# Performance work log

Measured on AMD Instinct MI355X. Metric: run time of the kernel, lower is better.

Reference implementation:

```python
import jax, jax.numpy as jnp
import numpy as np
import math

C_S = 256
NUM_HEADS = 8
HEAD_DIM = 32
TOTAL = NUM_HEADS * HEAD_DIM
B, S, I = 1, 256, 256  # batch, msa sequences (column attn axis), residues
LN_EPS = 1e-5


def setup_inputs() -> dict:
    key = jax.random.key(0)
    ks = jax.random.split(key, 10)
    sc = 1.0 / math.sqrt(C_S)
    return {
        "msa": jax.random.normal(ks[0], (B, S, I, C_S), dtype=jnp.float32),
        "ln_gamma": jnp.ones((C_S,), dtype=jnp.float32),
        "ln_beta": jnp.zeros((C_S,), dtype=jnp.float32),
        "Wq": jax.random.normal(ks[1], (C_S, TOTAL), dtype=jnp.float32) * sc,
        "Wk": jax.random.normal(ks[2], (C_S, TOTAL), dtype=jnp.float32) * sc,
        "Wv": jax.random.normal(ks[3], (C_S, TOTAL), dtype=jnp.float32) * sc,
        "Wg": jax.random.normal(ks[4], (C_S, TOTAL), dtype=jnp.float32) * sc,
        "bg": jnp.zeros((TOTAL,), dtype=jnp.float32),
        "Wo": jax.random.normal(ks[5], (TOTAL, C_S), dtype=jnp.float32) * (1.0 / math.sqrt(TOTAL)),
        "bo": jnp.zeros((C_S,), dtype=jnp.float32),
    }


def reference(msa, ln_gamma, ln_beta, Wq, Wk, Wv, Wg, bg, Wo, bo):
    # LayerNorm over channel dim
    mu = jnp.mean(msa, axis=-1, keepdims=True)
    var = jnp.mean(jnp.square(msa - mu), axis=-1, keepdims=True)
    x = (msa - mu) * jax.lax.rsqrt(var + LN_EPS) * ln_gamma + ln_beta

    b, s, i, _ = x.shape
    hd = (NUM_HEADS, HEAD_DIM)
    Q = (x @ Wq).reshape(b, s, i, *hd)
    K = (x @ Wk).reshape(b, s, i, *hd)
    V = (x @ Wv).reshape(b, s, i, *hd)
    G = jax.nn.sigmoid((x @ Wg + bg).reshape(b, s, i, *hd))

    # column attention: contract over head_dim, attend over sequence axis s/t
    scores = jnp.einsum('bsihd,btihd->bihst', Q, K) / math.sqrt(HEAD_DIM)
    attn = jax.nn.softmax(scores, axis=-1)
    vals = jnp.einsum('bihst,btihd->bsihd', attn, V)

    vals = (G * vals).reshape(b, s, i, TOTAL)
    return vals @ Wo + bo
```

## Files before the change

### kernel.cpp

```cpp
#include <hip/hip_runtime.h>
#include <hip/hip_fp16.h>
#include <math.h>

#define C_S 256
#define NUM_HEADS 8
#define HEAD_DIM 32
#define TOTAL 256
#define S_DIM 256
#define I_DIM 256
#define NROWS (S_DIM * I_DIM)
#define LN_EPS 1e-5f
#define QSCALE 0.25503534f

typedef _Float16 f16x8 __attribute__((ext_vector_type(8)));
typedef __attribute__((ext_vector_type(4))) float f32x4;

__device__ __forceinline__ ushort f2h(float x) {
  return __half_as_ushort(__float2half(x));
}
__device__ __forceinline__ float h2f(ushort u) {
  return __half2float(__ushort_as_half(u));
}
__device__ __forceinline__ uint pkrtz(float a, float b) {
  return __builtin_bit_cast(uint, __builtin_amdgcn_cvt_pkrtz(a, b));
}
__device__ __forceinline__ void gl16(const void* g, void* l) {
  __builtin_amdgcn_global_load_lds(
      (const __attribute__((address_space(1))) unsigned*)g,
      (__attribute__((address_space(3))) unsigned*)l, 16, 0, 0);
}
__device__ __forceinline__ void quadx(uint x0, uint x1, uint& o0, uint& o1) {
  auto a = __builtin_amdgcn_permlane32_swap(x0, x1, false, false);
  auto b = __builtin_amdgcn_permlane16_swap(a[0], a[1], false, false);
  o0 = b[0]; o1 = b[1];
}

__global__ __launch_bounds__(256) void prep_w_kernel(
    const float* __restrict__ Wq, const float* __restrict__ Wk,
    const float* __restrict__ Wv, const float* __restrict__ Wg,
    const float* __restrict__ Wo,
    ushort* __restrict__ Wch, ushort* __restrict__ Woh) {
  const int b = blockIdx.x;
  const int mat = b >> 8, n = b & 255;
  const int k = threadIdx.x;
  const float* W = (mat == 0) ? Wq : (mat == 1) ? Wk
                  : (mat == 2) ? Wv : (mat == 3) ? Wg : Wo;
  ushort h = f2h(W[(size_t)k * 256 + n]);
  if (mat < 4) Wch[((size_t)(mat * 256 + n)) * 256 + k] = h;
  else         Woh[(size_t)n * 256 + k] = h;
}

__global__ __launch_bounds__(256) void prep_x_kernel(
    const float* __restrict__ msa, const float* __restrict__ gamma,
    const float* __restrict__ beta, ushort* __restrict__ Xh) {
  const int row  = blockIdx.x * 4 + (threadIdx.x >> 6);
  const int lane = threadIdx.x & 63;
  float4 v = ((const float4*)(msa + (size_t)row * C_S))[lane];
  float sum = v.x + v.y + v.z + v.w;
  float sq  = v.x*v.x + v.y*v.y + v.z*v.z + v.w*v.w;
  #pragma unroll
  for (int off = 1; off < 64; off <<= 1) {
    sum += __shfl_xor(sum, off);
    sq  += __shfl_xor(sq, off);
  }
  float mu = sum * (1.0f / 256.0f);
  float rs = rsqrtf(sq * (1.0f / 256.0f) - mu * mu + LN_EPS);
  float4 gv = ((const float4*)gamma)[lane];
  float4 bv = ((const float4*)beta)[lane];
  ushort4 hh;
  hh.x = f2h((v.x - mu) * rs * gv.x + bv.x);
  hh.y = f2h((v.y - mu) * rs * gv.y + bv.y);
  hh.z = f2h((v.z - mu) * rs * gv.z + bv.z);
  hh.w = f2h((v.w - mu) * rs * gv.w + bv.w);
  *(ushort4*)(Xh + (size_t)row * 256 + lane * 4) = hh;
}

__global__ __launch_bounds__(256, 3) void fused_attn_kernel(
    const ushort* __restrict__ Xh,
    const ushort* __restrict__ Wch,
    const float* __restrict__ bg,
    ushort* __restrict__ Oh) {
  __shared__ __align__(16) ushort Kls[256][40];
  __shared__ __align__(16) ushort Vth[32][264];

  const int bid = blockIdx.x;
  const int xcd = bid & 7, j = bid >> 3;
  const int h = j & 7;
  const int i = (xcd << 5) + (j >> 3);
  const int ih = i * NUM_HEADS + h;
  const int tid = threadIdx.x;
  const int wave = tid >> 6, lane = tid & 63;
  const int lr = lane & 15, quad = lane >> 4;
  const int s_base = wave * 64;
  const size_t hbase = (size_t)ih * (S_DIM * HEAD_DIM);

  const ushort* xr0 = Xh + ((size_t)(s_base + lr) * 256 + i) * 256 + quad * 8;
  const ushort* wr0 = Wch + ((size_t)(h * 32 + lr)) * 256 + quad * 8;

  f32x4 kacc[2][4] = {}, vacc[2][4] = {};
  #pragma unroll
  for (int kb = 0; kb < 8; ++kb) {
    f16x8 xb[4];
    #pragma unroll
    for (int nt = 0; nt < 4; ++nt)
      xb[nt] = *(const f16x8*)(xr0 + (size_t)nt * 16 * 65536 + kb * 32);
    f16x8 wk[2], wv[2];
    #pragma unroll
    for (int mt = 0; mt < 2; ++mt) {
      wk[mt] = *(const f16x8*)(wr0 + (size_t)1 * 65536 + mt * 4096 + kb * 32);
      wv[mt] = *(const f16x8*)(wr0 + (size_t)2 * 65536 + mt * 4096 + kb * 32);
    }
    #pragma unroll
    for (int mt = 0; mt < 2; ++mt)
      #pragma unroll
      for (int nt = 0; nt < 4; ++nt) {
        kacc[mt][nt] = __builtin_amdgcn_mfma_f32_16x16x32_f16(wk[mt], xb[nt], kacc[mt][nt], 0, 0, 0);
        vacc[mt][nt] = __builtin_amdgcn_mfma_f32_16x16x32_f16(xb[nt], wv[mt], vacc[mt][nt], 0, 0, 0);
      }
  }
  #pragma unroll
  for (int mt = 0; mt < 2; ++mt)
    #pragma unroll
    for (int nt = 0; nt < 4; ++nt) {
      const int t = s_base + nt * 16 + lr;
      ushort4 kp;
      kp.x = f2h(kacc[mt][nt][0]); kp.y = f2h(kacc[mt][nt][1]);
      kp.z = f2h(kacc[mt][nt][2]); kp.w = f2h(kacc[mt][nt][3]);
      *(ushort4*)&Kls[t][mt * 16 + quad * 4] = kp;
      ushort4 vp;
      vp.x = f2h(vacc[mt][nt][0]); vp.y = f2h(vacc[mt][nt][1]);
      vp.z = f2h(vacc[mt][nt][2]); vp.w = f2h(vacc[mt][nt][3]);
      *(ushort4*)&Vth[mt * 16 + lr][s_base + nt * 16 + quad * 4] = vp;
    }

  f32x4 qacc[2][4] = {}, gacc[2][4] = {};
  #pragma unroll
  for (int kb = 0; kb < 8; ++kb) {
    f16x8 xb[4];
    #pragma unroll
    for (int nt = 0; nt < 4; ++nt)
      xb[nt] = *(const f16x8*)(xr0 + (size_t)nt * 16 * 65536 + kb * 32);
    f16x8 wq[2], wg[2];
    #pragma unroll
    for (int mt = 0; mt < 2; ++mt) {
      wq[mt] = *(const f16x8*)(wr0 + (size_t)0 * 65536 + mt * 4096 + kb * 32);
      wg[mt] = *(const f16x8*)(wr0 + (size_t)3 * 65536 + mt * 4096 + kb * 32);
    }
    #pragma unroll
    for (int mt = 0; mt < 2; ++mt)
      #pragma unroll
      for (int nt = 0; nt < 4; ++nt) {
        qacc[mt][nt] = __builtin_amdgcn_mfma_f32_16x16x32_f16(wq[mt], xb[nt], qacc[mt][nt], 0, 0, 0);
        gacc[mt][nt] = __builtin_amdgcn_mfma_f32_16x16x32_f16(wg[mt], xb[nt], gacc[mt][nt], 0, 0, 0);
      }
  }
  f16x8 qf[4];
  #pragma unroll
  for (int ns = 0; ns < 4; ++ns) {
    uint x0 = (uint)f2h(qacc[0][ns][0] * QSCALE) | ((uint)f2h(qacc[0][ns][1] * QSCALE) << 16);
    uint y0 = (uint)f2h(qacc[0][ns][2] * QSCALE) | ((uint)f2h(qacc[0][ns][3] * QSCALE) << 16);
    uint x1 = (uint)f2h(qacc[1][ns][0] * QSCALE) | ((uint)f2h(qacc[1][ns][1] * QSCALE) << 16);
    uint y1 = (uint)f2h(qacc[1][ns][2] * QSCALE) | ((uint)f2h(qacc[1][ns][3] * QSCALE) << 16);
    uint qa, qb, qc, qd2;
    quadx(x0, x1, qa, qb);
    quadx(y0, y1, qc, qd2);
    uint4 qw4 = make_uint4(qa, qc, qb, qd2);
    qf[ns] = __builtin_bit_cast(f16x8, qw4);
  }

  __syncthreads();

  f32x4 oacc[2][4] = {};
  float lpart[4] = {};
  #pragma unroll 1
  for (int c = 0; c < 4; ++c) {
    const int t0 = c * 64;
    #pragma unroll
    for (int half = 0; half < 2; ++half) {
      f16x8 kf0 = *(const f16x8*)&Kls[t0 + (half * 2 + 0) * 16 + lr][quad * 8];
      f16x8 kf1 = *(const f16x8*)&Kls[t0 + (half * 2 + 1) * 16 + lr][quad * 8];
      const int tq = t0 + half * 32 + quad * 8;
      f16x8 v0 = *(const f16x8*)&Vth[lr][tq];
      f16x8 v1 = *(const f16x8*)&Vth[16 + lr][tq];
      #pragma unroll
      for (int ns = 0; ns < 4; ++ns) {
        f32x4 s0 = {}, s1 = {};
        s0 = __builtin_amdgcn_mfma_f32_16x16x32_f16(kf0, qf[ns], s0, 0, 0, 0);
        s1 = __builtin_amdgcn_mfma_f32_16x16x32_f16(kf1, qf[ns], s1, 0, 0, 0);
        float e00 = exp2f(s0[0]), e01 = exp2f(s0[1]);
        float e02 = exp2f(s0[2]), e03 = exp2f(s0[3]);
        float e10 = exp2f(s1[0]), e11 = exp2f(s1[1]);
        float e12 = exp2f(s1[2]), e13 = exp2f(s1[3]);
        lpart[ns] += ((e00 + e01) + (e02 + e03)) + ((e10 + e11) + (e12 + e13));
        uint x0 = pkrtz(e00, e01), y0 = pkrtz(e02, e03);
        uint x1 = pkrtz(e10, e11), y1 = pkrtz(e12, e13);
        uint pa, pb, pc, pd;
        quadx(x0, x1, pa, pb);
        quadx(y0, y1, pc, pd);
        uint4 pw4 = make_uint4(pa, pc, pb, pd);
        f16x8 pf = __builtin_bit_cast(f16x8, pw4);
        __builtin_amdgcn_s_setprio(1);
        oacc[0][ns] = __builtin_amdgcn_mfma_f32_16x16x32_f16(v0, pf, oacc[0][ns], 0, 0, 0);
        oacc[1][ns] = __builtin_amdgcn_mfma_f32_16x16x32_f16(v1, pf, oacc[1][ns], 0, 0, 0);
        __builtin_amdgcn_s_setprio(0);
      }
    }
  }

  float invl[4];
  #pragma unroll
  for (int ns = 0; ns < 4; ++ns) {
    float v = lpart[ns];
    v += __shfl_xor(v, 16);
    v += __shfl_xor(v, 32);
    invl[ns] = 1.0f / v;
  }

  #pragma unroll
  for (int ns = 0; ns < 4; ++ns) {
    const int s = s_base + ns * 16 + lr;
    #pragma unroll
    for (int md = 0; md < 2; ++md) {
      const int d0 = md * 16 + quad * 4;
      float4 bgv = *(const float4*)(bg + h * 32 + d0);
      float g0 = 1.0f / (1.0f + __expf(-(gacc[md][ns][0] + bgv.x)));
      float g1 = 1.0f / (1.0f + __expf(-(gacc[md][ns][1] + bgv.y)));
      float g2 = 1.0f / (1.0f + __expf(-(gacc[md][ns][2] + bgv.z)));
      float g3 = 1.0f / (1.0f + __expf(-(gacc[md][ns][3] + bgv.w)));
      ushort4 ov;
      ov.x = f2h(g0 * oacc[md][ns][0] * invl[ns]);
      ov.y = f2h(g1 * oacc[md][ns][1] * invl[ns]);
      ov.z = f2h(g2 * oacc[md][ns][2] * invl[ns]);
      ov.w = f2h(g3 * oacc[md][ns][3] * invl[ns]);
      *(ushort4*)(Oh + hbase + (size_t)s * HEAD_DIM + d0) = ov;
    }
  }
}

__global__ __launch_bounds__(256) void out_kernel(
    const ushort* __restrict__ Oh, const ushort* __restrict__ Woh,
    const float* __restrict__ bo, float* __restrict__ out) {
  __shared__ __align__(16) ushort At0[128 * 32];
  __shared__ __align__(16) ushort At1[128 * 32];
  __shared__ __align__(16) ushort Bt0[128 * 32];
  __shared__ __align__(16) ushort Bt1[128 * 32];

  const int bid = blockIdx.x;
  const int xcd = bid & 7;
  const int j   = bid >> 3;
  const int ntile = j & 1;
  const int rg    = (xcd << 6) + (j >> 1);
  const int n0 = ntile * 128;
  const int s  = rg >> 1;
  const int i0 = (rg & 1) * 128;
  const int tid = threadIdx.x;
  const int wave = tid >> 6, lane = tid & 63;
  const int wm = wave >> 1, wn = wave & 1;
  const int lr = lane & 15, quad = lane >> 4;
  const int fsw = (quad ^ ((lr >> 1) & 3)) * 8;

  const int slot = wave * 64 + lane;
  const int row0 = slot >> 2;
  const int kc   = ((slot & 3) ^ ((row0 >> 1) & 3)) * 8;

  const ushort* pA = Oh + (size_t)(i0 + row0) * 65536 + (size_t)s * 32 + kc;
  const ushort* pB = Woh + (size_t)(n0 + row0) * 256 + kc;
  const int ld0 = wave * 512;
  const int ld1 = 2048 + wave * 512;

  f32x4 acc[4][4] = {};

  for (int kk = 0; kk < 4; ++kk) {
    __syncthreads();
    gl16(pA,               At0 + ld0); gl16(pA + (size_t)64 * 65536,        At0 + ld1);
    gl16(pA + 8192,        At1 + ld0); gl16(pA + (size_t)64 * 65536 + 8192, At1 + ld1);
    gl16(pB,               Bt0 + ld0); gl16(pB + 64 * 256,                  Bt0 + ld1);
    gl16(pB + 32,          Bt1 + ld0); gl16(pB + 64 * 256 + 32,             Bt1 + ld1);
    pA += 16384;
    pB += 64;
    __syncthreads();

    f16x8 a0[4], a1[4], b0[4], b1[4];
    #pragma unroll
    for (int mt = 0; mt < 4; ++mt) {
      const int off = (wm * 64 + mt * 16 + lr) * 32 + fsw;
      a0[mt] = *(const f16x8*)&At0[off];
      a1[mt] = *(const f16x8*)&At1[off];
    }
    #pragma unroll
    for (int nt = 0; nt < 4; ++nt) {
      const int off = (wn * 64 + nt * 16 + lr) * 32 + fsw;
      b0[nt] = *(const f16x8*)&Bt0[off];
      b1[nt] = *(const f16x8*)&Bt1[off];
    }
    #pragma unroll
    for (int mt = 0; mt < 4; ++mt)
      #pragma unroll
      for (int nt = 0; nt < 4; ++nt) {
        acc[mt][nt] = __builtin_amdgcn_mfma_f32_16x16x32_f16(a0[mt], b0[nt], acc[mt][nt], 0, 0, 0);
        acc[mt][nt] = __builtin_amdgcn_mfma_f32_16x16x32_f16(a1[mt], b1[nt], acc[mt][nt], 0, 0, 0);
      }
  }

  #pragma unroll
  for (int nt = 0; nt < 4; ++nt) {
    const int col = n0 + wn * 64 + nt * 16 + lr;
    const float b = bo[col];
    #pragma unroll
    for (int mt = 0; mt < 4; ++mt)
      #pragma unroll
      for (int reg = 0; reg < 4; ++reg) {
        const int mloc = wm * 64 + mt * 16 + quad * 4 + reg;
        out[((size_t)s * 256 + i0 + mloc) * C_S + col] = acc[mt][nt][reg] + b;
      }
  }
}

extern "C" void kernel_launch(void* const* d_in, const int* in_sizes, int n_in,
                              void* d_out, int out_size, void* d_ws, size_t ws_size,
                              hipStream_t stream) {
  const float* msa   = (const float*)d_in[0];
  const float* gamma = (const float*)d_in[1];
  const float* beta  = (const float*)d_in[2];
  const float* Wq    = (const float*)d_in[3];
  const float* Wk    = (const float*)d_in[4];
  const float* Wv    = (const float*)d_in[5];
  const float* Wg    = (const float*)d_in[6];
  const float* bg    = (const float*)d_in[7];
  const float* Wo    = (const float*)d_in[8];
  const float* bo    = (const float*)d_in[9];
  float* out = (float*)d_out;

  const size_t PLANE = (size_t)NROWS * TOTAL;
  ushort* Oh  = (ushort*)d_ws;
  ushort* Wch = Oh + PLANE;
  ushort* Woh = Wch + 1024 * 256;
  ushort* Xh = (ushort*)d_out;

  prep_w_kernel<<<1280, 256, 0, stream>>>(Wq, Wk, Wv, Wg, Wo, Wch, Woh);
  prep_x_kernel<<<NROWS / 4, 256, 0, stream>>>(msa, gamma, beta, Xh);
  fused_attn_kernel<<<I_DIM * NUM_HEADS, 256, 0, stream>>>(Xh, Wch, bg, Oh);
  out_kernel<<<1024, 256, 0, stream>>>(Oh, Woh, bo, out);
}
```

Baseline: 286.2 us.

## Spill sigmoid gate to global scratch to cut registers and raise occupancy

After: 289.8 us. No clear change (+1.3%).

```diff
diff --git a/kernel.cpp b/kernel.cpp
--- a/kernel.cpp
+++ b/kernel.cpp
@@ -75,11 +75,12 @@
   *(ushort4*)(Xh + (size_t)row * 256 + lane * 4) = hh;
 }
 
-__global__ __launch_bounds__(256, 3) void fused_attn_kernel(
+__global__ __launch_bounds__(256, 4) void fused_attn_kernel(
     const ushort* __restrict__ Xh,
     const ushort* __restrict__ Wch,
     const float* __restrict__ bg,
-    ushort* __restrict__ Oh) {
+    ushort* __restrict__ Oh,
+    ushort* __restrict__ Gh) {
   __shared__ __align__(16) ushort Kls[256][40];
   __shared__ __align__(16) ushort Vth[32][264];
 
@@ -97,75 +98,94 @@
   const ushort* xr0 = Xh + ((size_t)(s_base + lr) * 256 + i) * 256 + quad * 8;
   const ushort* wr0 = Wch + ((size_t)(h * 32 + lr)) * 256 + quad * 8;
 
-  f32x4 kacc[2][4] = {}, vacc[2][4] = {};
-  #pragma unroll
-  for (int kb = 0; kb < 8; ++kb) {
-    f16x8 xb[4];
-    #pragma unroll
-    for (int nt = 0; nt < 4; ++nt)
-      xb[nt] = *(const f16x8*)(xr0 + (size_t)nt * 16 * 65536 + kb * 32);
-    f16x8 wk[2], wv[2];
+  {
+    f32x4 kacc[2][4] = {}, vacc[2][4] = {};
+    #pragma unroll
+    for (int kb = 0; kb < 8; ++kb) {
+      f16x8 xb[4];
+      #pragma unroll
+      for (int nt = 0; nt < 4; ++nt)
+        xb[nt] = *(const f16x8*)(xr0 + (size_t)nt * 16 * 65536 + kb * 32);
+      f16x8 wk[2], wv[2];
+      #pragma unroll
+      for (int mt = 0; mt < 2; ++mt) {
+        wk[mt] = *(const f16x8*)(wr0 + (size_t)1 * 65536 + mt * 4096 + kb * 32);
+        wv[mt] = *(const f16x8*)(wr0 + (size_t)2 * 65536 + mt * 4096 + kb * 32);
+      }
+      #pragma unroll
+      for (int mt = 0; mt < 2; ++mt)
+        #pragma unroll
+        for (int nt = 0; nt < 4; ++nt) {
+          kacc[mt][nt] = __builtin_amdgcn_mfma_f32_16x16x32_f16(wk[mt], xb[nt], kacc[mt][nt], 0, 0, 0);
+          vacc[mt][nt] = __builtin_amdgcn_mfma_f32_16x16x32_f16(xb[nt], wv[mt], vacc[mt][nt], 0, 0, 0);
+        }
+    }
+    #pragma unroll
+    for (int mt = 0; mt < 2; ++mt)
+      #pragma unroll
+      for (int nt = 0; nt < 4; ++nt) {
+        const int t = s_base + nt * 16 + lr;
+        ushort4 kp;
+        kp.x = f2h(kacc[mt][nt][0]); kp.y = f2h(kacc[mt][nt][1]);
+        kp.z = f2h(kacc[mt][nt][2]); kp.w = f2h(kacc[mt][nt][3]);
+        *(ushort4*)&Kls[t][mt * 16 + quad * 4] = kp;
+        ushort4 vp;
+        vp.x = f2h(vacc[mt][nt][0]); vp.y = f2h(vacc[mt][nt][1]);
+        vp.z = f2h(vacc[mt][nt][2]); vp.w = f2h(vacc[mt][nt][3]);
+        *(ushort4*)&Vth[mt * 16 + lr][s_base + nt * 16 + quad * 4] = vp;
+      }
+  }
+
+  f16x8 qf[4];
+  {
+    f32x4 qacc[2][4] = {}, gacc[2][4] = {};
+    #pragma unroll
+    for (int kb = 0; kb < 8; ++kb) {
+      f16x8 xb[4];
+      #pragma unroll
+      for (int nt = 0; nt < 4; ++nt)
+        xb[nt] = *(const f16x8*)(xr0 + (size_t)nt * 16 * 65536 + kb * 32);
+      f16x8 wq[2], wg[2];
+      #pragma unroll
+      for (int mt = 0; mt < 2; ++mt) {
+        wq[mt] = *(const f16x8*)(wr0 + (size_t)0 * 65536 + mt * 4096 + kb * 32);
+        wg[mt] = *(const f16x8*)(wr0 + (size_t)3 * 65536 + mt * 4096 + kb * 32);
+      }
+      #pragma unroll
+      for (int mt = 0; mt < 2; ++mt)
+        #pragma unroll
+        for (int nt = 0; nt < 4; ++nt) {
+          qacc[mt][nt] = __builtin_amdgcn_mfma_f32_16x16x32_f16(wq[mt], xb[nt], qacc[mt][nt], 0, 0, 0);
+          gacc[mt][nt] = __builtin_amdgcn_mfma_f32_16x16x32_f16(wg[mt], xb[nt], gacc[mt][nt], 0, 0, 0);
+        }
+    }
     #pragma unroll
     for (int mt = 0; mt < 2; ++mt) {
-      wk[mt] = *(const f16x8*)(wr0 + (size_t)1 * 65536 + mt * 4096 + kb * 32);
-      wv[mt] = *(const f16x8*)(wr0 + (size_t)2 * 65536 + mt * 4096 + kb * 32);
-    }
-    #pragma unroll
-    for (int mt = 0; mt < 2; ++mt)
+      const int d0 = mt * 16 + quad * 4;
+      float4 bgv = *(const float4*)(bg + h * 32 + d0);
       #pragma unroll
       for (int nt = 0; nt < 4; ++nt) {
-        kacc[mt][nt] = __builtin_amdgcn_mfma_f32_16x16x32_f16(wk[mt], xb[nt], kacc[mt][nt], 0, 0, 0);
-        vacc[mt][nt] = __builtin_amdgcn_mfma_f32_16x16x32_f16(xb[nt], wv[mt], vacc[mt][nt], 0, 0, 0);
-      }
-  }
-  #pragma unroll
-  for (int mt = 0; mt < 2; ++mt)
-    #pragma unroll
-    for (int nt = 0; nt < 4; ++nt) {
-      const int t = s_base + nt * 16 + lr;
-      ushort4 kp;
-      kp.x = f2h(kacc[mt][nt][0]); kp.y = f2h(kacc[mt][nt][1]);
-      kp.z = f2h(kacc[mt][nt][2]); kp.w = f2h(kacc[mt][nt][3]);
-      *(ushort4*)&Kls[t][mt * 16 + quad * 4] = kp;
-      ushort4 vp;
-      vp.x = f2h(vacc[mt][nt][0]); vp.y = f2h(vacc[mt][nt][1]);
-      vp.z = f2h(vacc[mt][nt][2]); vp.w = f2h(vacc[mt][nt][3]);
-      *(ushort4*)&Vth[mt * 16 + lr][s_base + nt * 16 + quad * 4] = vp;
-    }
-
-  f32x4 qacc[2][4] = {}, gacc[2][4] = {};
-  #pragma unroll
-  for (int kb = 0; kb < 8; ++kb) {
-    f16x8 xb[4];
-    #pragma unroll
-    for (int nt = 0; nt < 4; ++nt)
-      xb[nt] = *(const f16x8*)(xr0 + (size_t)nt * 16 * 65536 + kb * 32);
-    f16x8 wq[2], wg[2];
-    #pragma unroll
-    for (int mt = 0; mt < 2; ++mt) {
-      wq[mt] = *(const f16x8*)(wr0 + (size_t)0 * 65536 + mt * 4096 + kb * 32);
-      wg[mt] = *(const f16x8*)(wr0 + (size_t)3 * 65536 + mt * 4096 + kb * 32);
-    }
-    #pragma unroll
-    for (int mt = 0; mt < 2; ++mt)
-      #pragma unroll
-      for (int nt = 0; nt < 4; ++nt) {
-        qacc[mt][nt] = __builtin_amdgcn_mfma_f32_16x16x32_f16(wq[mt], xb[nt], qacc[mt][nt], 0, 0, 0);
-        gacc[mt][nt] = __builtin_amdgcn_mfma_f32_16x16x32_f16(wg[mt], xb[nt], gacc[mt][nt], 0, 0, 0);
-      }
-  }
-  f16x8 qf[4];
-  #pragma unroll
-  for (int ns = 0; ns < 4; ++ns) {
-    uint x0 = (uint)f2h(qacc[0][ns][0] * QSCALE) | ((uint)f2h(qacc[0][ns][1] * QSCALE) << 16);
-    uint y0 = (uint)f2h(qacc[0][ns][2] * QSCALE) | ((uint)f2h(qacc[0][ns][3] * QSCALE) << 16);
-    uint x1 = (uint)f2h(qacc[1][ns][0] * QSCALE) | ((uint)f2h(qacc[1][ns][1] * QSCALE) << 16);
-    uint y1 = (uint)f2h(qacc[1][ns][2] * QSCALE) | ((uint)f2h(qacc[1][ns][3] * QSCALE) << 16);
-    uint qa, qb, qc, qd2;
-    quadx(x0, x1, qa, qb);
-    quadx(y0, y1, qc, qd2);
-    uint4 qw4 = make_uint4(qa, qc, qb, qd2);
-    qf[ns] = __builtin_bit_cast(f16x8, qw4);
+        const int s = s_base + nt * 16 + lr;
+        ushort4 gp;
+        gp.x = f2h(1.0f / (1.0f + __expf(-(gacc[mt][nt][0] + bgv.x))));
+        gp.y = f2h(1.0f / (1.0f + __expf(-(gacc[mt][nt][1] + bgv.y))));
+        gp.z = f2h(1.0f / (1.0f + __expf(-(gacc[mt][nt][2] + bgv.z))));
+        gp.w = f2h(1.0f / (1.0f + __expf(-(gacc[mt][nt][3] + bgv.w))));
+        *(ushort4*)(Gh + hbase + (size_t)s * HEAD_DIM + d0) = gp;
+      }
+    }
+    #pragma unroll
+    for (int ns = 0; ns < 4; ++ns) {
+      uint x0 = (uint)f2h(qacc[0][ns][0] * QSCALE) | ((uint)f2h(qacc[0][ns][1] * QSCALE) << 16);
+      uint y0 = (uint)f2h(qacc[0][ns][2] * QSCALE) | ((uint)f2h(qacc[0][ns][3] * QSCALE) << 16);
+      uint x1 = (uint)f2h(qacc[1][ns][0] * QSCALE) | ((uint)f2h(qacc[1][ns][1] * QSCALE) << 16);
+      uint y1 = (uint)f2h(qacc[1][ns][2] * QSCALE) | ((uint)f2h(qacc[1][ns][3] * QSCALE) << 16);
+      uint qa, qb, qc, qd2;
+      quadx(x0, x1, qa, qb);
+      quadx(y0, y1, qc, qd2);
+      uint4 qw4 = make_uint4(qa, qc, qb, qd2);
+      qf[ns] = __builtin_bit_cast(f16x8, qw4);
+    }
   }
 
   __syncthreads();
@@ -199,10 +219,8 @@
         quadx(y0, y1, pc, pd);
         uint4 pw4 = make_uint4(pa, pc, pb, pd);
         f16x8 pf = __builtin_bit_cast(f16x8, pw4);
-        __builtin_amdgcn_s_setprio(1);
         oacc[0][ns] = __builtin_amdgcn_mfma_f32_16x16x32_f16(v0, pf, oacc[0][ns], 0, 0, 0);
         oacc[1][ns] = __builtin_amdgcn_mfma_f32_16x16x32_f16(v1, pf, oacc[1][ns], 0, 0, 0);
-        __builtin_amdgcn_s_setprio(0);
       }
     }
   }
@@ -222,16 +240,12 @@
     #pragma unroll
     for (int md = 0; md < 2; ++md) {
       const int d0 = md * 16 + quad * 4;
-      float4 bgv = *(const float4*)(bg + h * 32 + d0);
-      float g0 = 1.0f / (1.0f + __expf(-(gacc[md][ns][0] + bgv.x)));
-      float g1 = 1.0f / (1.0f + __expf(-(gacc[md][ns][1] + bgv.y)));
-      float g2 = 1.0f / (1.0f + __expf(-(gacc[md][ns][2] + bgv.z)));
-      float g3 = 1.0f / (1.0f + __expf(-(gacc[md][ns][3] + bgv.w)));
+      ushort4 g4 = *(const ushort4*)(Gh + hbase + (size_t)s * HEAD_DIM + d0);
       ushort4 ov;
-      ov.x = f2h(g0 * oacc[md][ns][0] * invl[ns]);
-      ov.y = f2h(g1 * oacc[md][ns][1] * invl[ns]);
-      ov.z = f2h(g2 * oacc[md][ns][2] * invl[ns]);
-      ov.w = f2h(g3 * oacc[md][ns][3] * invl[ns]);
+      ov.x = f2h(h2f(g4.x) * oacc[md][ns][0] * invl[ns]);
+      ov.y = f2h(h2f(g4.y) * oacc[md][ns][1] * invl[ns]);
+      ov.z = f2h(h2f(g4.z) * oacc[md][ns][2] * invl[ns]);
+      ov.w = f2h(h2f(g4.w) * oacc[md][ns][3] * invl[ns]);
       *(ushort4*)(Oh + hbase + (size_t)s * HEAD_DIM + d0) = ov;
     }
   }
@@ -336,9 +350,10 @@
   ushort* Wch = Oh + PLANE;
   ushort* Woh = Wch + 1024 * 256;
   ushort* Xh = (ushort*)d_out;
+  ushort* Gh = Xh + PLANE;
 
   prep_w_kernel<<<1280, 256, 0, stream>>>(Wq, Wk, Wv, Wg, Wo, Wch, Woh);
   prep_x_kernel<<<NROWS / 4, 256, 0, stream>>>(msa, gamma, beta, Xh);
-  fused_attn_kernel<<<I_DIM * NUM_HEADS, 256, 0, stream>>>(Xh, Wch, bg, Oh);
+  fused_attn_kernel<<<I_DIM * NUM_HEADS, 256, 0, stream>>>(Xh, Wch, bg, Oh, Gh);
   out_kernel<<<1024, 256, 0, stream>>>(Oh, Woh, bo, out);
 }
```

## Double-buffer LDS loads in output projection GEMM with async prefetch

Applied to the files above, without the earlier changes.

After: 281.8 us. About the same (-1.5%).

```diff
diff --git a/kernel.cpp b/kernel.cpp
--- a/kernel.cpp
+++ b/kernel.cpp
@@ -240,10 +240,8 @@
 __global__ __launch_bounds__(256) void out_kernel(
     const ushort* __restrict__ Oh, const ushort* __restrict__ Woh,
     const float* __restrict__ bo, float* __restrict__ out) {
-  __shared__ __align__(16) ushort At0[128 * 32];
-  __shared__ __align__(16) ushort At1[128 * 32];
-  __shared__ __align__(16) ushort Bt0[128 * 32];
-  __shared__ __align__(16) ushort Bt1[128 * 32];
+  __shared__ __align__(16) ushort As[2][128 * 32];
+  __shared__ __align__(16) ushort Bs[2][128 * 32];
 
   const int bid = blockIdx.x;
   const int xcd = bid & 7;
@@ -270,37 +268,45 @@
 
   f32x4 acc[4][4] = {};
 
-  for (int kk = 0; kk < 4; ++kk) {
-    __syncthreads();
-    gl16(pA,               At0 + ld0); gl16(pA + (size_t)64 * 65536,        At0 + ld1);
-    gl16(pA + 8192,        At1 + ld0); gl16(pA + (size_t)64 * 65536 + 8192, At1 + ld1);
-    gl16(pB,               Bt0 + ld0); gl16(pB + 64 * 256,                  Bt0 + ld1);
-    gl16(pB + 32,          Bt1 + ld0); gl16(pB + 64 * 256 + 32,             Bt1 + ld1);
-    pA += 16384;
-    pB += 64;
-    __syncthreads();
-
-    f16x8 a0[4], a1[4], b0[4], b1[4];
-    #pragma unroll
-    for (int mt = 0; mt < 4; ++mt) {
-      const int off = (wm * 64 + mt * 16 + lr) * 32 + fsw;
-      a0[mt] = *(const f16x8*)&At0[off];
-      a1[mt] = *(const f16x8*)&At1[off];
-    }
-    #pragma unroll
-    for (int nt = 0; nt < 4; ++nt) {
-      const int off = (wn * 64 + nt * 16 + lr) * 32 + fsw;
-      b0[nt] = *(const f16x8*)&Bt0[off];
-      b1[nt] = *(const f16x8*)&Bt1[off];
-    }
+  #define STAGE(buf, kk)                                                     \
+    do {                                                                     \
+      const ushort* a_ = pA + (size_t)(kk) * 8192;                           \
+      const ushort* b_ = pB + (kk) * 32;                                     \
+      gl16(a_,                      As[buf] + ld0);                          \
+      gl16(a_ + (size_t)64 * 65536, As[buf] + ld1);                          \
+      gl16(b_,                      Bs[buf] + ld0);                          \
+      gl16(b_ + 64 * 256,           Bs[buf] + ld1);                          \
+    } while (0)
+
+  STAGE(0, 0);
+  int cur = 0;
+  #pragma unroll 1
+  for (int kk = 0; kk < 8; ++kk) {
+    if (kk < 7) {
+      STAGE(cur ^ 1, kk + 1);
+      asm volatile("s_waitcnt vmcnt(4)" ::: "memory");
+    } else {
+      asm volatile("s_waitcnt vmcnt(0)" ::: "memory");
+    }
+    __builtin_amdgcn_s_barrier();
+
+    f16x8 a0[4], b0[4];
     #pragma unroll
     for (int mt = 0; mt < 4; ++mt)
-      #pragma unroll
-      for (int nt = 0; nt < 4; ++nt) {
+      a0[mt] = *(const f16x8*)&As[cur][(wm * 64 + mt * 16 + lr) * 32 + fsw];
+    #pragma unroll
+    for (int nt = 0; nt < 4; ++nt)
+      b0[nt] = *(const f16x8*)&Bs[cur][(wn * 64 + nt * 16 + lr) * 32 + fsw];
+    #pragma unroll
+    for (int mt = 0; mt < 4; ++mt)
+      #pragma unroll
+      for (int nt = 0; nt < 4; ++nt)
         acc[mt][nt] = __builtin_amdgcn_mfma_f32_16x16x32_f16(a0[mt], b0[nt], acc[mt][nt], 0, 0, 0);
-        acc[mt][nt] = __builtin_amdgcn_mfma_f32_16x16x32_f16(a1[mt], b1[nt], acc[mt][nt], 0, 0, 0);
-      }
-  }
+
+    __builtin_amdgcn_s_barrier();
+    cur ^= 1;
+  }
+  #undef STAGE
 
   #pragma unroll
   for (int nt = 0; nt < 4; ++nt) {
```
